# Kernel optimization log

Hardware: AMD Instinct MI355X
Metric: run time of the kernel (lower is better)

Reference implementation:

```python
import jax, jax.numpy as jnp
import numpy as np

TEMPERATURE = 0.07
WEIGHT = 0.5
EPS = 1e-8  # torch CosineSimilarity eps


def setup_inputs() -> dict:
    key = jax.random.key(0)
    k1, k2 = jax.random.split(key)
    N, D = 16384, 256
    img_features = jax.random.normal(k1, (N, D), dtype=jnp.float32)
    txt_features = jax.random.normal(k2, (N, D), dtype=jnp.float32)
    return {"img_features": img_features, "txt_features": txt_features}


def _l2_normalize(x):
    # matches torch cosine_similarity: clamp each norm to EPS
    n = jnp.sqrt(jnp.sum(x * x, axis=-1, keepdims=True))
    return x / jnp.maximum(n, EPS)


def reference(img_features, txt_features):
    v = _l2_normalize(img_features)  # [N, D]
    u = _l2_normalize(txt_features)  # [N, D]
    # cosine-sim matrix via GEMM (same math as broadcasted CosineSimilarity)
    sim_vu = jnp.einsum('nd,md->nm', v, u) / TEMPERATURE  # [N, N]
    sim_uv = sim_vu.T  # cosine similarity is symmetric in its args
    N = sim_vu.shape[0]
    diag = jnp.arange(N)
    # CrossEntropyLoss with targets = arange(N): mean over rows of -log_softmax[i, i]
    logp_vu = jax.nn.log_softmax(sim_vu, axis=-1)
    logp_uv = jax.nn.log_softmax(sim_uv, axis=-1)
    loss_vu = -jnp.mean(logp_vu[diag, diag])
    loss_uv = -jnp.mean(logp_uv[diag, diag])
    total = WEIGHT * loss_vu + (1.0 - WEIGHT) * loss_uv
    # corresponds to {'T': total, 'I-T': loss_vu, 'T-I': loss_uv}
    return jnp.stack([total, loss_vu, loss_uv])
```

## Files before the change

### kernel.cpp

```cpp
#include <hip/hip_runtime.h>
#include <hip/hip_bf16.h>


#define D_DIM 256

constexpr float INV_T = 1.0f / 0.07f;
constexpr float EXP2_SCALE = 1.44269504088896340736f / 0.07f;

typedef __bf16 bf16x8 __attribute__((ext_vector_type(8)));
typedef float f32x4 __attribute__((ext_vector_type(4)));

__global__ __launch_bounds__(256) void normalize_kernel(
    const float* __restrict__ img, const float* __restrict__ txt,
    __hip_bfloat16* __restrict__ Vf, __hip_bfloat16* __restrict__ Uf,
    float* __restrict__ diagarr, float* __restrict__ rowsum,
    float* __restrict__ colsum, float* __restrict__ partials) {
  const int wave = threadIdx.x >> 6;
  const int lane = threadIdx.x & 63;
  const int sub = lane >> 5;
  const int pos = lane & 31;
  const int row = blockIdx.x * 8 + wave * 2 + sub;
  const size_t base = (size_t)row * D_DIM + pos * 8;

  const float4 i0 = *reinterpret_cast<const float4*>(&img[base]);
  const float4 i1 = *reinterpret_cast<const float4*>(&img[base + 4]);
  const float4 t0 = *reinterpret_cast<const float4*>(&txt[base]);
  const float4 t1 = *reinterpret_cast<const float4*>(&txt[base + 4]);

  float a = i0.x * i0.x + i0.y * i0.y + i0.z * i0.z + i0.w * i0.w +
            i1.x * i1.x + i1.y * i1.y + i1.z * i1.z + i1.w * i1.w;
  float b = t0.x * t0.x + t0.y * t0.y + t0.z * t0.z + t0.w * t0.w +
            t1.x * t1.x + t1.y * t1.y + t1.z * t1.z + t1.w * t1.w;
#pragma unroll
  for (int off = 1; off < 32; off <<= 1) {
    a += __shfl_xor(a, off, 64);
    b += __shfl_xor(b, off, 64);
  }
  const float si = 1.0f / fmaxf(sqrtf(a), 1e-8f);
  const float st = 1.0f / fmaxf(sqrtf(b), 1e-8f);

  const float vs = si * EXP2_SCALE;
  __hip_bfloat16 vb8[8] = {
      __float2bfloat16(i0.x * vs), __float2bfloat16(i0.y * vs),
      __float2bfloat16(i0.z * vs), __float2bfloat16(i0.w * vs),
      __float2bfloat16(i1.x * vs), __float2bfloat16(i1.y * vs),
      __float2bfloat16(i1.z * vs), __float2bfloat16(i1.w * vs)};
  __hip_bfloat16 ub8[8] = {
      __float2bfloat16(t0.x * st), __float2bfloat16(t0.y * st),
      __float2bfloat16(t0.z * st), __float2bfloat16(t0.w * st),
      __float2bfloat16(t1.x * st), __float2bfloat16(t1.y * st),
      __float2bfloat16(t1.z * st), __float2bfloat16(t1.w * st)};

  const int g = row >> 4, l15r = row & 15;
  const int ks = pos >> 2, quad = pos & 3;
  const size_t foff = (size_t)(g * 8 + ks) * 512 + (quad * 16 + l15r) * 8;
  *reinterpret_cast<uint4*>(&Vf[foff]) = *reinterpret_cast<uint4*>(vb8);
  *reinterpret_cast<uint4*>(&Uf[foff]) = *reinterpret_cast<uint4*>(ub8);

  float d = (i0.x * si) * (t0.x * st) + (i0.y * si) * (t0.y * st) +
            (i0.z * si) * (t0.z * st) + (i0.w * si) * (t0.w * st) +
            (i1.x * si) * (t1.x * st) + (i1.y * si) * (t1.y * st) +
            (i1.z * si) * (t1.z * st) + (i1.w * si) * (t1.w * st);
#pragma unroll
  for (int off = 1; off < 32; off <<= 1) d += __shfl_xor(d, off, 64);
  if (pos == 0) diagarr[row] = d;

  if (threadIdx.x < 8) {
    rowsum[blockIdx.x * 8 + threadIdx.x] = 0.0f;
    colsum[blockIdx.x * 8 + threadIdx.x] = 0.0f;
  }
  if (blockIdx.x == 0 && threadIdx.x < 4) partials[threadIdx.x] = 0.0f;
}

__global__ __launch_bounds__(512, 2) void gemm_lse_kernel(
    const __hip_bfloat16* __restrict__ Vf, const __hip_bfloat16* __restrict__ Uf,
    float* __restrict__ rowsum, float* __restrict__ colsum, int n) {
  __shared__ float colbuf[8192];

  const int tid = threadIdx.x;
  const int lane = tid & 63;
  const int w = tid >> 6;
  const int quad = lane >> 4;
  const int l15 = lane & 15;
  const int rb = blockIdx.x >> 1;
  const int ch = blockIdx.x & 1;
  const int njt = n >> 10;
  const int jt0 = ch * njt;

  bf16x8 a[4][8];
#pragma unroll
  for (int mi = 0; mi < 4; ++mi)
#pragma unroll
    for (int ks = 0; ks < 8; ++ks)
      a[mi][ks] = *reinterpret_cast<const bf16x8*>(
          Vf + (size_t)((4 * rb + mi) * 8 + ks) * 512 + lane * 8);

  float rs[4][4] = {};

  const __hip_bfloat16* Ub = Uf + (size_t)(w * 4) * 8 * 512 + lane * 8;
  const size_t jstart = (size_t)jt0 * (32 * 8 * 512);

  bf16x8 bb[2][4];
#pragma unroll
  for (int ni = 0; ni < 4; ++ni)
    bb[0][ni] =
        *reinterpret_cast<const bf16x8*>(Ub + jstart + (size_t)(ni * 8) * 512);

  for (int jl = 0; jl < njt; ++jl) {
    const size_t jb = jstart + (size_t)jl * (32 * 8 * 512);
    const size_t jbn = (jl < njt - 1) ? jb + 32 * 8 * 512 : jstart;
    f32x4 acc[4][4] = {};

#pragma unroll
    for (int ks = 0; ks < 8; ++ks) {
      {
        const size_t pjb = (ks < 7) ? jb : jbn;
        const int pks = (ks < 7) ? ks + 1 : 0;
#pragma unroll
        for (int ni = 0; ni < 4; ++ni)
          bb[(ks + 1) & 1][ni] = *reinterpret_cast<const bf16x8*>(
              Ub + pjb + (size_t)(ni * 8 + pks) * 512);
        __builtin_amdgcn_sched_barrier(0);
      }
#pragma unroll
      for (int mi = 0; mi < 4; ++mi)
#pragma unroll
        for (int ni = 0; ni < 4; ++ni)
          acc[mi][ni] = __builtin_amdgcn_mfma_f32_16x16x32_bf16(
              a[mi][ks], bb[ks & 1][ni], acc[mi][ni], 0, 0, 0);
    }

    float cs0 = 0.f, cs1 = 0.f, cs2 = 0.f, cs3 = 0.f;
#pragma unroll
    for (int mi = 0; mi < 4; ++mi)
#pragma unroll
      for (int r = 0; r < 4; ++r) {
        const float e0 = __builtin_amdgcn_exp2f(acc[mi][0][r]);
        const float e1 = __builtin_amdgcn_exp2f(acc[mi][1][r]);
        const float e2 = __builtin_amdgcn_exp2f(acc[mi][2][r]);
        const float e3 = __builtin_amdgcn_exp2f(acc[mi][3][r]);
        rs[mi][r] += e0 + e1 + e2 + e3;
        cs0 += e0; cs1 += e1; cs2 += e2; cs3 += e3;
      }
    float csa[4] = {cs0, cs1, cs2, cs3};
#pragma unroll
    for (int ni = 0; ni < 4; ++ni) {
      float c = csa[ni];
      c += __shfl_xor(c, 16, 64);
      c += __shfl_xor(c, 32, 64);
      if (lane < 16)
        colbuf[jl * 512 + w * 64 + ni * 16 + l15] = c;
    }
  }

  __syncthreads();
  const int colbase = ch * (n >> 1);
  for (int i = tid; i < (n >> 1); i += 512)
    atomicAdd(&colsum[colbase + i], colbuf[i]);

#pragma unroll
  for (int mi = 0; mi < 4; ++mi)
#pragma unroll
    for (int r = 0; r < 4; ++r) {
      float v = rs[mi][r];
      v += __shfl_xor(v, 1, 64);
      v += __shfl_xor(v, 2, 64);
      v += __shfl_xor(v, 4, 64);
      v += __shfl_xor(v, 8, 64);
      if (l15 == 0)
        atomicAdd(&rowsum[rb * 64 + mi * 16 + quad * 4 + r], v);
    }
}

__global__ __launch_bounds__(256) void finalize_partial(
    const float* __restrict__ rowsum, const float* __restrict__ colsum,
    const float* __restrict__ diagarr, float* __restrict__ partials, int n) {
  float sr = 0.0f, sc = 0.0f, sd = 0.0f;
  for (int i = blockIdx.x * 256 + threadIdx.x; i < n; i += gridDim.x * 256) {
    sr += __logf(rowsum[i]);
    sc += __logf(colsum[i]);
    sd += diagarr[i];
  }
#pragma unroll
  for (int off = 1; off < 64; off <<= 1) {
    sr += __shfl_xor(sr, off, 64);
    sc += __shfl_xor(sc, off, 64);
    sd += __shfl_xor(sd, off, 64);
  }
  if ((threadIdx.x & 63) == 0) {
    atomicAdd(&partials[0], sr);
    atomicAdd(&partials[1], sc);
    atomicAdd(&partials[2], sd);
  }
}

__global__ void finalize_final(const float* __restrict__ partials,
                               float* __restrict__ out, int n) {
  const float invN = 1.0f / (float)n;
  const float dm = partials[2] * INV_T * invN;
  const float lvu = partials[0] * invN - dm;
  const float luv = partials[1] * invN - dm;
  out[0] = 0.5f * lvu + 0.5f * luv;
  out[1] = lvu;
  out[2] = luv;
}

extern "C" void kernel_launch(void* const* d_in, const int* in_sizes, int n_in,
                              void* d_out, int out_size, void* d_ws, size_t ws_size,
                              hipStream_t stream) {
  const float* img = (const float*)d_in[0];
  const float* txt = (const float*)d_in[1];
  float* out = (float*)d_out;
  const int N = in_sizes[0] / D_DIM;

  char* ws = (char*)d_ws;
  __hip_bfloat16* Vf = (__hip_bfloat16*)ws;
  __hip_bfloat16* Uf = (__hip_bfloat16*)(ws + (size_t)N * D_DIM * 2);
  float* rowsum = (float*)(ws + (size_t)N * D_DIM * 4);
  float* colsum = rowsum + N;
  float* diagarr = colsum + N;
  float* partials = diagarr + N;

  normalize_kernel<<<N / 8, 256, 0, stream>>>(img, txt, Vf, Uf, diagarr,
                                              rowsum, colsum, partials);

  gemm_lse_kernel<<<N / 32, 512, 0, stream>>>(Vf, Uf, rowsum, colsum, N);

  finalize_partial<<<64, 256, 0, stream>>>(rowsum, colsum, diagarr, partials,
                                           N);
  finalize_final<<<1, 1, 0, stream>>>(partials, out, N);
}
```

Measured before the change: 236.9 us.

## Software-pipeline exp2 epilogue with MFMA via ping-pong half-tile accumulators

Splits each wave's 4 column tiles into two halves with separate accumulator sets (accA/accB) and interleaves the exp2/row-column-sum epilogue of the previous half into the MFMA loop of the current half. The goal is to hide transcendental and reduction work behind matrix-core execution instead of running it serially after each tile. Register pressure stays similar (two 4x2 accumulator sets instead of one 4x4), but the control flow and the indexing are more intricate. There is also a risk of scheduling conflicts from the sched_barrier placement.

```diff
diff --git a/kernel.cpp b/kernel.cpp
--- a/kernel.cpp
+++ b/kernel.cpp
@@ -85,7 +85,6 @@
   const int rb = blockIdx.x >> 1;
   const int ch = blockIdx.x & 1;
   const int njt = n >> 10;
-  const int jt0 = ch * njt;
 
   bf16x8 a[4][8];
 #pragma unroll
@@ -97,59 +96,94 @@
 
   float rs[4][4] = {};
 
-  const __hip_bfloat16* Ub = Uf + (size_t)(w * 4) * 8 * 512 + lane * 8;
-  const size_t jstart = (size_t)jt0 * (32 * 8 * 512);
-
-  bf16x8 bb[2][4];
-#pragma unroll
-  for (int ni = 0; ni < 4; ++ni)
-    bb[0][ni] =
-        *reinterpret_cast<const bf16x8*>(Ub + jstart + (size_t)(ni * 8) * 512);
+  const __hip_bfloat16* Ub = Uf + lane * 8;
+  const size_t PH = (size_t)8 * 512;
+  const size_t gbase0 = ((size_t)ch * 512 + w * 4) * PH;
+
+  bf16x8 bb[2][2];
+  f32x4 accA[4][2], accB[4][2];
+  const f32x4 fz = {};
+
+#define PHASE(ACC, GCUR, GNEXT, EPI, EACC, CBASE)                           \
+  {                                                                         \
+    float ecs0 = 0.f, ecs1 = 0.f;                                           \
+    _Pragma("unroll") for (int ks = 0; ks < 8; ++ks) {                      \
+      {                                                                     \
+        const size_t pg = (ks < 7) ? (GCUR) : (GNEXT);                      \
+        const int pks = (ks < 7) ? ks + 1 : 0;                              \
+        bb[(ks + 1) & 1][0] = *reinterpret_cast<const bf16x8*>(             \
+            Ub + pg + (size_t)pks * 512);                                   \
+        bb[(ks + 1) & 1][1] = *reinterpret_cast<const bf16x8*>(             \
+            Ub + pg + PH + (size_t)pks * 512);                              \
+        __builtin_amdgcn_sched_barrier(0);                                  \
+      }                                                                     \
+      _Pragma("unroll") for (int mi = 0; mi < 4; ++mi) {                    \
+        ACC[mi][0] = __builtin_amdgcn_mfma_f32_16x16x32_bf16(               \
+            a[mi][ks], bb[ks & 1][0], (ks == 0) ? fz : ACC[mi][0], 0, 0, 0);\
+        ACC[mi][1] = __builtin_amdgcn_mfma_f32_16x16x32_bf16(               \
+            a[mi][ks], bb[ks & 1][1], (ks == 0) ? fz : ACC[mi][1], 0, 0, 0);\
+      }                                                                     \
+      if (EPI) {                                                            \
+        const int emi = ks >> 1, er = (ks & 1) * 2;                         \
+        _Pragma("unroll") for (int rr = 0; rr < 2; ++rr) {                  \
+          const float e0 = __builtin_amdgcn_exp2f(EACC[emi][0][er + rr]);   \
+          const float e1 = __builtin_amdgcn_exp2f(EACC[emi][1][er + rr]);   \
+          rs[emi][er + rr] += e0 + e1;                                      \
+          ecs0 += e0;                                                       \
+          ecs1 += e1;                                                       \
+        }                                                                   \
+      }                                                                     \
+    }                                                                       \
+    if (EPI) {                                                              \
+      ecs0 += __shfl_xor(ecs0, 16, 64);                                     \
+      ecs0 += __shfl_xor(ecs0, 32, 64);                                     \
+      ecs1 += __shfl_xor(ecs1, 16, 64);                                     \
+      ecs1 += __shfl_xor(ecs1, 32, 64);                                     \
+      if (lane < 16) {                                                      \
+        colbuf[(CBASE) + l15] = ecs0;                                       \
+        colbuf[(CBASE) + 16 + l15] = ecs1;                                  \
+      }                                                                     \
+    }                                                                       \
+  }
+
+  bb[0][0] = *reinterpret_cast<const bf16x8*>(Ub + gbase0);
+  bb[0][1] = *reinterpret_cast<const bf16x8*>(Ub + gbase0 + PH);
+
+  PHASE(accA, gbase0, gbase0 + 2 * PH, 0, accA, 0);
 
   for (int jl = 0; jl < njt; ++jl) {
-    const size_t jb = jstart + (size_t)jl * (32 * 8 * 512);
-    const size_t jbn = (jl < njt - 1) ? jb + 32 * 8 * 512 : jstart;
-    f32x4 acc[4][4] = {};
-
-#pragma unroll
-    for (int ks = 0; ks < 8; ++ks) {
-      {
-        const size_t pjb = (ks < 7) ? jb : jbn;
-        const int pks = (ks < 7) ? ks + 1 : 0;
-#pragma unroll
-        for (int ni = 0; ni < 4; ++ni)
-          bb[(ks + 1) & 1][ni] = *reinterpret_cast<const bf16x8*>(
-              Ub + pjb + (size_t)(ni * 8 + pks) * 512);
-        __builtin_amdgcn_sched_barrier(0);
+    const size_t g0 = gbase0 + ((size_t)jl * 32) * PH;
+    const size_t g1 = g0 + 2 * PH;
+    const size_t gn0 = (jl < njt - 1) ? g0 + 32 * PH : g1;
+    const size_t gn1 = gn0 + 2 * PH;
+    const int cb = jl * 512 + w * 64;
+
+    PHASE(accB, g1, gn0, 1, accA, cb);
+    if (jl < njt - 1) {
+      PHASE(accA, gn0, gn1, 1, accB, cb + 32);
+    }
+  }
+
+  {
+    float ecs0 = 0.f, ecs1 = 0.f;
+#pragma unroll
+    for (int mi = 0; mi < 4; ++mi)
+#pragma unroll
+      for (int r = 0; r < 4; ++r) {
+        const float e0 = __builtin_amdgcn_exp2f(accB[mi][0][r]);
+        const float e1 = __builtin_amdgcn_exp2f(accB[mi][1][r]);
+        rs[mi][r] += e0 + e1;
+        ecs0 += e0;
+        ecs1 += e1;
       }
-#pragma unroll
-      for (int mi = 0; mi < 4; ++mi)
-#pragma unroll
-        for (int ni = 0; ni < 4; ++ni)
-          acc[mi][ni] = __builtin_amdgcn_mfma_f32_16x16x32_bf16(
-              a[mi][ks], bb[ks & 1][ni], acc[mi][ni], 0, 0, 0);
-    }
-
-    float cs0 = 0.f, cs1 = 0.f, cs2 = 0.f, cs3 = 0.f;
-#pragma unroll
-    for (int mi = 0; mi < 4; ++mi)
-#pragma unroll
-      for (int r = 0; r < 4; ++r) {
-        const float e0 = __builtin_amdgcn_exp2f(acc[mi][0][r]);
-        const float e1 = __builtin_amdgcn_exp2f(acc[mi][1][r]);
-        const float e2 = __builtin_amdgcn_exp2f(acc[mi][2][r]);
-        const float e3 = __builtin_amdgcn_exp2f(acc[mi][3][r]);
-        rs[mi][r] += e0 + e1 + e2 + e3;
-        cs0 += e0; cs1 += e1; cs2 += e2; cs3 += e3;
-      }
-    float csa[4] = {cs0, cs1, cs2, cs3};
-#pragma unroll
-    for (int ni = 0; ni < 4; ++ni) {
-      float c = csa[ni];
-      c += __shfl_xor(c, 16, 64);
-      c += __shfl_xor(c, 32, 64);
-      if (lane < 16)
-        colbuf[jl * 512 + w * 64 + ni * 16 + l15] = c;
+    ecs0 += __shfl_xor(ecs0, 16, 64);
+    ecs0 += __shfl_xor(ecs0, 32, 64);
+    ecs1 += __shfl_xor(ecs1, 16, 64);
+    ecs1 += __shfl_xor(ecs1, 32, 64);
+    const int cb = (njt - 1) * 512 + w * 64 + 32;
+    if (lane < 16) {
+      colbuf[cb + l15] = ecs0;
+      colbuf[cb + 16 + l15] = ecs1;
     }
   }
 
```

Result: slower. 320.6 us (+35.3%).

## Switch GEMM to 32x32x16 MFMA with matching fragment layout

Applied to the files above, without the earlier changes.

Replaces the 16x16x32 bf16 MFMA tiling with 32x32x16 MFMA and rewrites the pre-packed fragment layout that normalize_kernel writes so each 32-row group is stored with 16 k-steps. Each wave now computes a 2x2 grid of 32x32 tiles instead of a 4x4 grid of 16x16 tiles. This cuts the number of MFMA instructions and B-fragment loads per k-step, and the epilogue reductions are reworked for the 32x32 accumulator layout. The risk is higher accumulator register pressure (f32x16) and subtle row-index mapping errors in the rowsum atomics.

```diff
diff --git a/kernel.cpp b/kernel.cpp
--- a/kernel.cpp
+++ b/kernel.cpp
@@ -8,7 +8,7 @@
 constexpr float EXP2_SCALE = 1.44269504088896340736f / 0.07f;
 
 typedef __bf16 bf16x8 __attribute__((ext_vector_type(8)));
-typedef float f32x4 __attribute__((ext_vector_type(4)));
+typedef float f32x16 __attribute__((ext_vector_type(16)));
 
 __global__ __launch_bounds__(256) void normalize_kernel(
     const float* __restrict__ img, const float* __restrict__ txt,
@@ -51,9 +51,9 @@
       __float2bfloat16(t1.x * st), __float2bfloat16(t1.y * st),
       __float2bfloat16(t1.z * st), __float2bfloat16(t1.w * st)};
 
-  const int g = row >> 4, l15r = row & 15;
-  const int ks = pos >> 2, quad = pos & 3;
-  const size_t foff = (size_t)(g * 8 + ks) * 512 + (quad * 16 + l15r) * 8;
+  const int g32 = row >> 5, m = row & 31;
+  const int ks = pos >> 1, h = pos & 1;
+  const size_t foff = (size_t)(g32 * 16 + ks) * 512 + (h * 32 + m) * 8;
   *reinterpret_cast<uint4*>(&Vf[foff]) = *reinterpret_cast<uint4*>(vb8);
   *reinterpret_cast<uint4*>(&Uf[foff]) = *reinterpret_cast<uint4*>(ub8);
 
@@ -80,76 +80,77 @@
   const int tid = threadIdx.x;
   const int lane = tid & 63;
   const int w = tid >> 6;
-  const int quad = lane >> 4;
-  const int l15 = lane & 15;
+  const int l31 = lane & 31;
+  const int h = lane >> 5;
   const int rb = blockIdx.x >> 1;
   const int ch = blockIdx.x & 1;
   const int njt = n >> 10;
-  const int jt0 = ch * njt;
-
-  bf16x8 a[4][8];
-#pragma unroll
-  for (int mi = 0; mi < 4; ++mi)
-#pragma unroll
-    for (int ks = 0; ks < 8; ++ks)
+
+  bf16x8 a[2][16];
+#pragma unroll
+  for (int mi = 0; mi < 2; ++mi)
+#pragma unroll
+    for (int ks = 0; ks < 16; ++ks)
       a[mi][ks] = *reinterpret_cast<const bf16x8*>(
-          Vf + (size_t)((4 * rb + mi) * 8 + ks) * 512 + lane * 8);
-
-  float rs[4][4] = {};
-
-  const __hip_bfloat16* Ub = Uf + (size_t)(w * 4) * 8 * 512 + lane * 8;
-  const size_t jstart = (size_t)jt0 * (32 * 8 * 512);
-
-  bf16x8 bb[2][4];
-#pragma unroll
-  for (int ni = 0; ni < 4; ++ni)
-    bb[0][ni] =
-        *reinterpret_cast<const bf16x8*>(Ub + jstart + (size_t)(ni * 8) * 512);
+          Vf + (size_t)((2 * rb + mi) * 16 + ks) * 512 + lane * 8);
+
+  float rs[2][16] = {};
+
+  const __hip_bfloat16* Ub = Uf + lane * 8;
+  const size_t PH = (size_t)16 * 512;
+  const size_t gbase0 = ((size_t)ch * 256 + w * 2) * PH;
+  const size_t JSTRIDE = 16 * PH;
+
+  bf16x8 bb[2][2];
+  f32x16 acc[2][2];
+
+  bb[0][0] = *reinterpret_cast<const bf16x8*>(Ub + gbase0);
+  bb[0][1] = *reinterpret_cast<const bf16x8*>(Ub + gbase0 + PH);
 
   for (int jl = 0; jl < njt; ++jl) {
-    const size_t jb = jstart + (size_t)jl * (32 * 8 * 512);
-    const size_t jbn = (jl < njt - 1) ? jb + 32 * 8 * 512 : jstart;
-    f32x4 acc[4][4] = {};
-
-#pragma unroll
-    for (int ks = 0; ks < 8; ++ks) {
+    const size_t jb = gbase0 + (size_t)jl * JSTRIDE;
+    const size_t jbn = (jl < njt - 1) ? jb + JSTRIDE : gbase0;
+#pragma unroll
+    for (int mi = 0; mi < 2; ++mi)
+#pragma unroll
+      for (int ni = 0; ni < 2; ++ni)
+        acc[mi][ni] = (f32x16){};
+
+#pragma unroll
+    for (int ks = 0; ks < 16; ++ks) {
       {
-        const size_t pjb = (ks < 7) ? jb : jbn;
-        const int pks = (ks < 7) ? ks + 1 : 0;
-#pragma unroll
-        for (int ni = 0; ni < 4; ++ni)
-          bb[(ks + 1) & 1][ni] = *reinterpret_cast<const bf16x8*>(
-              Ub + pjb + (size_t)(ni * 8 + pks) * 512);
+        const size_t pjb = (ks < 15) ? jb : jbn;
+        const int pks = (ks < 15) ? ks + 1 : 0;
+        bb[(ks + 1) & 1][0] = *reinterpret_cast<const bf16x8*>(
+            Ub + pjb + (size_t)pks * 512);
+        bb[(ks + 1) & 1][1] = *reinterpret_cast<const bf16x8*>(
+            Ub + pjb + PH + (size_t)pks * 512);
         __builtin_amdgcn_sched_barrier(0);
       }
 #pragma unroll
-      for (int mi = 0; mi < 4; ++mi)
-#pragma unroll
-        for (int ni = 0; ni < 4; ++ni)
-          acc[mi][ni] = __builtin_amdgcn_mfma_f32_16x16x32_bf16(
+      for (int mi = 0; mi < 2; ++mi)
+#pragma unroll
+        for (int ni = 0; ni < 2; ++ni)
+          acc[mi][ni] = __builtin_amdgcn_mfma_f32_32x32x16_bf16(
               a[mi][ks], bb[ks & 1][ni], acc[mi][ni], 0, 0, 0);
     }
 
-    float cs0 = 0.f, cs1 = 0.f, cs2 = 0.f, cs3 = 0.f;
-#pragma unroll
-    for (int mi = 0; mi < 4; ++mi)
-#pragma unroll
-      for (int r = 0; r < 4; ++r) {
-        const float e0 = __builtin_amdgcn_exp2f(acc[mi][0][r]);
-        const float e1 = __builtin_amdgcn_exp2f(acc[mi][1][r]);
-        const float e2 = __builtin_amdgcn_exp2f(acc[mi][2][r]);
-        const float e3 = __builtin_amdgcn_exp2f(acc[mi][3][r]);
-        rs[mi][r] += e0 + e1 + e2 + e3;
-        cs0 += e0; cs1 += e1; cs2 += e2; cs3 += e3;
+    float cs0 = 0.f, cs1 = 0.f;
+#pragma unroll
+    for (int mi = 0; mi < 2; ++mi)
+#pragma unroll
+      for (int reg = 0; reg < 16; ++reg) {
+        const float e0 = __builtin_amdgcn_exp2f(acc[mi][0][reg]);
+        const float e1 = __builtin_amdgcn_exp2f(acc[mi][1][reg]);
+        rs[mi][reg] += e0 + e1;
+        cs0 += e0;
+        cs1 += e1;
       }
-    float csa[4] = {cs0, cs1, cs2, cs3};
-#pragma unroll
-    for (int ni = 0; ni < 4; ++ni) {
-      float c = csa[ni];
-      c += __shfl_xor(c, 16, 64);
-      c += __shfl_xor(c, 32, 64);
-      if (lane < 16)
-        colbuf[jl * 512 + w * 64 + ni * 16 + l15] = c;
+    cs0 += __shfl_xor(cs0, 32, 64);
+    cs1 += __shfl_xor(cs1, 32, 64);
+    if (lane < 32) {
+      colbuf[jl * 512 + w * 64 + l31] = cs0;
+      colbuf[jl * 512 + w * 64 + 32 + l31] = cs1;
     }
   }
 
@@ -159,16 +160,19 @@
     atomicAdd(&colsum[colbase + i], colbuf[i]);
 
 #pragma unroll
-  for (int mi = 0; mi < 4; ++mi)
-#pragma unroll
-    for (int r = 0; r < 4; ++r) {
-      float v = rs[mi][r];
+  for (int mi = 0; mi < 2; ++mi)
+#pragma unroll
+    for (int reg = 0; reg < 16; ++reg) {
+      float v = rs[mi][reg];
       v += __shfl_xor(v, 1, 64);
       v += __shfl_xor(v, 2, 64);
       v += __shfl_xor(v, 4, 64);
       v += __shfl_xor(v, 8, 64);
-      if (l15 == 0)
-        atomicAdd(&rowsum[rb * 64 + mi * 16 + quad * 4 + r], v);
+      v += __shfl_xor(v, 16, 64);
+      if (l31 == 0) {
+        const int r = (reg & 3) + 8 * (reg >> 2) + 4 * h;
+        atomicAdd(&rowsum[rb * 64 + mi * 32 + r], v);
+      }
     }
 }
 
```

Result: slower. 243.1 us (+2.6%).
